# Optimization experiments

Measured on AMD Instinct MI355X. Metric: run time of the kernel, lower is better.

## Reference

```python
import jax, jax.numpy as jnp
import numpy as np

B, N, D_MODEL, H = 2, 2048, 1024, 16
HD = D_MODEL // H  # head_dim = 64

def setup_inputs() -> dict:
    key = jax.random.key(0)
    ks = jax.random.split(key, 5)
    x = jax.random.normal(ks[0], (B, N, D_MODEL), dtype=jnp.float32)
    scale = 0.02
    # Linear weights stored as [in, out] (torch does x @ W.T with W [out,in]; equivalent math)
    Wq = jax.random.normal(ks[1], (D_MODEL, D_MODEL), dtype=jnp.float32) * scale
    Wk = jax.random.normal(ks[2], (D_MODEL, D_MODEL), dtype=jnp.float32) * scale
    Wv = jax.random.normal(ks[3], (D_MODEL, D_MODEL), dtype=jnp.float32) * scale
    Wo = jax.random.normal(ks[4], (D_MODEL, D_MODEL), dtype=jnp.float32) * scale
    return {"x": x, "Wq": Wq, "Wk": Wk, "Wv": Wv, "Wo": Wo}

def reference(x, Wq, Wk, Wv, Wo):
    b, n, _ = x.shape
    # QKV projections (no bias; qkv_bias=False)
    q = (x @ Wq).reshape(b, n, H, HD)
    k = (x @ Wk).reshape(b, n, H, HD)
    v = (x @ Wv).reshape(b, n, H, HD)
    # scores [b, h, q, k]
    scores = jnp.einsum('bqhd,bkhd->bhqk', q, k) / jnp.sqrt(jnp.float32(HD))
    causal = jnp.triu(jnp.ones((n, n), dtype=bool), k=1)  # True above diagonal -> masked
    scores = jnp.where(causal, -jnp.inf, scores)
    attn = jax.nn.softmax(scores, axis=-1)  # dropout p=0.0 -> identity
    ctx = jnp.einsum('bhqk,bkhd->bqhd', attn, v).reshape(b, n, D_MODEL)
    return ctx @ Wo
```

## Files before the change

kernel.cpp:

```cpp
#include <hip/hip_runtime.h>
#include <math.h>

#define D_MODEL 1024
#define NHEAD 16
#define HD 64
#define SEQ 2048
#define BATCH 2
#define MTOT (BATCH * SEQ)

typedef __attribute__((ext_vector_type(8))) short bf16x8;
typedef __attribute__((ext_vector_type(4))) float f32x4;

__device__ __forceinline__ unsigned short f2bf(float f) {
    unsigned int u = __float_as_uint(f);
    u += 0x7FFF + ((u >> 16) & 1);
    return (unsigned short)(u >> 16);
}

__device__ __forceinline__ unsigned int pk2bf(float a, float b) {
    unsigned int r;
    asm("v_cvt_pk_bf16_f32 %0, %1, %2" : "=v"(r) : "v"(a), "v"(b));
    return r;
}

__device__ __forceinline__ void async16(unsigned short* lds, const unsigned short* g) {
    __builtin_amdgcn_global_load_lds(
        (const __attribute__((address_space(1))) unsigned int*)g,
        (__attribute__((address_space(3))) unsigned int*)lds, 16, 0, 0);
}

__device__ __forceinline__ void BAR() {
    asm volatile("" ::: "memory");
    __builtin_amdgcn_s_barrier();
    asm volatile("" ::: "memory");
}

__global__ __launch_bounds__(256) void prep(const float* __restrict__ x,
                                            unsigned short* __restrict__ xb,
                                            const float* __restrict__ W0,
                                            const float* __restrict__ W1,
                                            const float* __restrict__ W2,
                                            const float* __restrict__ W3,
                                            unsigned short* __restrict__ Wt) {
    const int bid = blockIdx.x;
    const int tid = threadIdx.x;
    if (bid < 4096) {
        const int i = (bid * 256 + tid) * 4;
        float4 v = *(const float4*)(x + i);
        uint2 pk;
        pk.x = pk2bf(v.x, v.y);
        pk.y = pk2bf(v.z, v.w);
        *(uint2*)(xb + i) = pk;
    } else {
        __shared__ float T[32][33];
        const int t = bid - 4096;
        const int z = t >> 10, rem = t & 1023;
        const int n0 = (rem & 31) * 32, k0 = (rem >> 5) * 32;
        const float* W = (z == 0) ? W0 : (z == 1) ? W1 : (z == 2) ? W2 : W3;
        unsigned short* out = Wt + (size_t)z * D_MODEL * D_MODEL;
        const int tx = tid & 31, ty = tid >> 5;
#pragma unroll
        for (int i = 0; i < 4; ++i)
            T[ty + 8 * i][tx] = W[(size_t)(k0 + ty + 8 * i) * D_MODEL + n0 + tx];
        __syncthreads();
#pragma unroll
        for (int i = 0; i < 4; ++i)
            out[(size_t)(n0 + ty + 8 * i) * D_MODEL + k0 + tx] = f2bf(T[tx][ty + 8 * i]);
    }
}

__global__ __launch_bounds__(512, 2) void qkv_mfma(const unsigned short* __restrict__ A,
                                                   const unsigned short* __restrict__ Wt,
                                                   unsigned short* __restrict__ q,
                                                   unsigned short* __restrict__ k,
                                                   unsigned short* __restrict__ vt) {
    __shared__ unsigned short SM[65536];
    const int tid = threadIdx.x;
    const int wave = tid >> 6, lane = tid & 63;
    const int quad = lane >> 4, l16 = lane & 15;
    const int wm = wave >> 2, wn = wave & 3;

    const int bid = blockIdx.x;
    const int swz = (bid & 7) * 24 + (bid >> 3);
    const int by = swz / 12, bx = swz % 12;
    const int m0 = by * 256;
    const int z = bx >> 2, c0 = (bx & 3) * 256;
    const unsigned short* Bz = Wt + (size_t)z * D_MODEL * D_MODEL;

    const unsigned short* aptr[2];
    const unsigned short* bptr[2];
    int ldsoff[2];
#pragma unroll
    for (int j = 0; j < 2; ++j) {
        const int s = j * 512 + tid;
        const int r = s >> 2;
        const int cg = (s & 3) ^ ((r + (r >> 2)) & 3);
        aptr[j] = A + (size_t)(m0 + r) * D_MODEL + cg * 8;
        bptr[j] = Bz + (size_t)(c0 + r) * D_MODEL + cg * 8;
        ldsoff[j] = (j * 512 + wave * 64) * 8;
    }

    const int key = (l16 + (l16 >> 2)) & 3;
    const int chunk = quad ^ key;
    int aoff[8], boff[4];
#pragma unroll
    for (int mt = 0; mt < 8; ++mt)
        aoff[mt] = ((wm * 128 + mt * 16 + l16) * 4 + chunk) * 8;
#pragma unroll
    for (int nt = 0; nt < 4; ++nt)
        boff[nt] = 16384 + ((wn * 64 + nt * 16 + l16) * 4 + chunk) * 8;

    f32x4 acc[8][4];
#pragma unroll
    for (int mt = 0; mt < 8; ++mt)
#pragma unroll
        for (int nt = 0; nt < 4; ++nt)
            acc[mt][nt] = (f32x4){0.f, 0.f, 0.f, 0.f};

    auto stage = [&](int d, int op, int ks, int T) {
        const int base = d * 32768 + op * 16384 + ks * 8192;
#pragma unroll
        for (int j = 0; j < 2; ++j)
            async16(SM + base + ldsoff[j],
                    (op ? bptr[j] : aptr[j]) + T * 64 + ks * 32);
    };
    auto dsA = [&](bf16x8* af, int mh, int d, int ks) {
        const int base = d * 32768 + ks * 8192;
#pragma unroll
        for (int i = 0; i < 4; ++i)
            af[i] = *(const bf16x8*)&SM[base + aoff[mh * 4 + i]];
    };
    auto dsB = [&](bf16x8* bf, int d, int ks) {
        const int base = d * 32768 + ks * 8192;
#pragma unroll
        for (int i = 0; i < 4; ++i)
            bf[i] = *(const bf16x8*)&SM[base + boff[i]];
    };
    auto mfma16 = [&](bf16x8* af, bf16x8* bf, int mh) {
        __builtin_amdgcn_s_setprio(1);
#pragma unroll
        for (int i = 0; i < 4; ++i)
#pragma unroll
            for (int nt = 0; nt < 4; ++nt)
                acc[mh * 4 + i][nt] = __builtin_amdgcn_mfma_f32_16x16x32_bf16(
                    af[i], bf[nt], acc[mh * 4 + i][nt], 0, 0, 0);
        __builtin_amdgcn_s_setprio(0);
    };

    stage(0, 0, 0, 0);
    stage(0, 1, 0, 0);
    stage(0, 0, 1, 0);
    stage(0, 1, 1, 0);
    asm volatile("s_waitcnt vmcnt(4)" ::: "memory");
    BAR();

    const int NT = D_MODEL / 64;
    for (int T = 0; T < NT; ++T) {
        const int d = T & 1, dn = d ^ 1;
        const bool nx = (T + 1 < NT);
        bf16x8 af[4], bf[4];
        if (nx) stage(dn, 0, 0, T + 1);
        dsA(af, 0, d, 0);
        dsB(bf, d, 0);
        mfma16(af, bf, 0);
        BAR();
        if (nx) stage(dn, 1, 0, T + 1);
        dsA(af, 1, d, 0);
        mfma16(af, bf, 1);
        if (nx) asm volatile("s_waitcnt vmcnt(4)" ::: "memory");
        else    asm volatile("s_waitcnt vmcnt(0)" ::: "memory");
        BAR();
        if (nx) stage(dn, 0, 1, T + 1);
        dsA(af, 0, d, 1);
        dsB(bf, d, 1);
        mfma16(af, bf, 0);
        BAR();
        if (nx) stage(dn, 1, 1, T + 1);
        dsA(af, 1, d, 1);
        mfma16(af, bf, 1);
        if (nx) asm volatile("s_waitcnt vmcnt(4)" ::: "memory");
        else    asm volatile("s_waitcnt vmcnt(0)" ::: "memory");
        BAR();
    }

    __syncthreads();
    const int bb = m0 >> 11, tok0 = m0 & (SEQ - 1), h0 = c0 >> 6;
    if (z < 2) {
        const float qsc = (z == 0) ? 0.18033688011112042f : 1.0f;
        unsigned short* dst = (z == 0) ? q : k;
#pragma unroll
        for (int pass = 0; pass < 2; ++pass) {
            if (pass) __syncthreads();
            if (wm == pass) {
#pragma unroll
                for (int mt = 0; mt < 8; ++mt)
#pragma unroll
                    for (int nt = 0; nt < 4; ++nt)
#pragma unroll
                        for (int reg = 0; reg < 4; ++reg) {
                            const int rr = mt * 16 + quad * 4 + reg;
                            const int cc = wn * 64 + nt * 16 + l16;
                            SM[rr * 264 + cc] = f2bf(acc[mt][nt][reg] * qsc);
                        }
            }
            __syncthreads();
#pragma unroll
            for (int it = 0; it < 8; ++it) {
                const int g = it * 512 + tid;
                const int r = g >> 5, gg = g & 31;
                uint4 val = *(const uint4*)&SM[r * 264 + gg * 8];
                *(uint4*)(dst + (((size_t)bb * NHEAD + h0 + (gg >> 3)) * SEQ +
                                 tok0 + pass * 128 + r) * HD + (gg & 7) * 8) = val;
            }
        }
    } else {
#pragma unroll
        for (int pass = 0; pass < 2; ++pass) {
            if (pass) __syncthreads();
            if (wm == pass) {
#pragma unroll
                for (int mt = 0; mt < 8; ++mt)
#pragma unroll
                    for (int nt = 0; nt < 4; ++nt) {
                        const int dd = wn * 64 + nt * 16 + l16;
                        const int m = mt * 16 + quad * 4;
                        uint2 w;
                        w.x = pk2bf(acc[mt][nt][0], acc[mt][nt][1]);
                        w.y = pk2bf(acc[mt][nt][2], acc[mt][nt][3]);
                        *(uint2*)&SM[dd * 136 + m] = w;
                    }
            }
            __syncthreads();
#pragma unroll
            for (int it = 0; it < 8; ++it) {
                const int g = it * 512 + tid;
                const int dd = g >> 4, tg = (g & 15) * 8;
                uint4 val = *(const uint4*)&SM[dd * 136 + tg];
                *(uint4*)(vt + (((size_t)bb * NHEAD + h0 + (dd >> 6)) * HD + (dd & 63)) * SEQ +
                          tok0 + pass * 128 + tg) = val;
            }
        }
    }
}

__global__ __launch_bounds__(256) void gemm_out(const unsigned short* __restrict__ A,
                                                const unsigned short* __restrict__ Bw,
                                                float* __restrict__ outf) {
    __shared__ unsigned short SM[16384];
    const int tid = threadIdx.x;
    const int m0 = blockIdx.y * 128, n0 = blockIdx.x * 128;
    const int wave = tid >> 6, lane = tid & 63;
    const int quad = lane >> 4, l16 = lane & 15;
    const int wm = wave & 1, wn = wave >> 1;

    f32x4 acc[4][4];
#pragma unroll
    for (int mt = 0; mt < 4; ++mt)
#pragma unroll
        for (int nt = 0; nt < 4; ++nt)
            acc[mt][nt] = (f32x4){0.f, 0.f, 0.f, 0.f};

    for (int k0 = 0; k0 < D_MODEL; k0 += 64) {
        __syncthreads();
#pragma unroll
        for (int i = 0; i < 4; ++i) {
            const int c = i * 256 + tid;
            const int r = c >> 3, cc = (c & 7) * 8;
            const int cbase = i * 256 + wave * 64;
            async16(SM + cbase * 8, A + (size_t)(m0 + r) * D_MODEL + k0 + cc);
            async16(SM + 8192 + cbase * 8, Bw + (size_t)(n0 + r) * D_MODEL + k0 + cc);
        }
        __syncthreads();
#pragma unroll
        for (int ks = 0; ks < 2; ++ks) {
            bf16x8 af[4], bfr[4];
#pragma unroll
            for (int mt = 0; mt < 4; ++mt)
                af[mt] = *(const bf16x8*)&SM[(wm * 64 + mt * 16 + l16) * 64 + ks * 32 + quad * 8];
#pragma unroll
            for (int nt = 0; nt < 4; ++nt)
                bfr[nt] = *(const bf16x8*)&SM[8192 + (wn * 64 + nt * 16 + l16) * 64 + ks * 32 + quad * 8];
#pragma unroll
            for (int mt = 0; mt < 4; ++mt)
#pragma unroll
                for (int nt = 0; nt < 4; ++nt)
                    acc[mt][nt] = __builtin_amdgcn_mfma_f32_16x16x32_bf16(
                        af[mt], bfr[nt], acc[mt][nt], 0, 0, 0);
        }
    }

#pragma unroll
    for (int mt = 0; mt < 4; ++mt)
#pragma unroll
        for (int nt = 0; nt < 4; ++nt)
#pragma unroll
            for (int reg = 0; reg < 4; ++reg) {
                const int m = m0 + wm * 64 + mt * 16 + quad * 4 + reg;
                const int n = n0 + wn * 64 + nt * 16 + l16;
                outf[(size_t)m * D_MODEL + n] = acc[mt][nt][reg];
            }
}

__global__ __launch_bounds__(256, 2) void attn_mfma(const unsigned short* __restrict__ Q,
                                                    const unsigned short* __restrict__ K,
                                                    const unsigned short* __restrict__ VT,
                                                    unsigned short* __restrict__ ctx) {
    __shared__ float CMB[8832];
    const int tid = threadIdx.x;
    const int wave = tid >> 6, lane = tid & 63;
    const int quad = lane >> 4, l16 = lane & 15;
    const int h = blockIdx.x, b = blockIdx.z;
    const int y = blockIdx.y;
    const unsigned short* Qp = Q + ((size_t)b * NHEAD + h) * SEQ * HD;
    const unsigned short* Kp = K + ((size_t)b * NHEAD + h) * SEQ * HD;
    const unsigned short* Vp = VT + ((size_t)b * NHEAD + h) * HD * SEQ;
    unsigned short* Pw = (unsigned short*)CMB + wave * 4096;
    const int sw8 = l16 & 7;

#pragma unroll 1
    for (int half = 0; half < 2; ++half) {
        const int p = half ? y : (31 - y);
        const int row0 = p * 64;
        if (half) __syncthreads();

        bf16x8 bQ[4][2];
#pragma unroll
        for (int f = 0; f < 4; ++f)
#pragma unroll
            for (int ks = 0; ks < 2; ++ks)
                bQ[f][ks] = *(const bf16x8*)(Qp +
                    (size_t)(row0 + f * 16 + l16) * HD + ks * 32 + quad * 8);

        f32x4 o[4][4];
        float ps[4] = {0.f, 0.f, 0.f, 0.f};
#pragma unroll
        for (int nt = 0; nt < 4; ++nt)
#pragma unroll
            for (int f = 0; f < 4; ++f)
                o[nt][f] = (f32x4){0.f, 0.f, 0.f, 0.f};

        for (int kt = wave; kt <= p; kt += 4) {
            bf16x8 aK[4][2];
#pragma unroll
            for (int mt = 0; mt < 4; ++mt)
#pragma unroll
                for (int ks = 0; ks < 2; ++ks)
                    aK[mt][ks] = *(const bf16x8*)(Kp +
                        (size_t)(kt * 64 + mt * 16 + l16) * HD + ks * 32 + quad * 8);

            f32x4 sT[4][4];
            __builtin_amdgcn_s_setprio(1);
#pragma unroll
            for (int mt = 0; mt < 4; ++mt)
#pragma unroll
                for (int f = 0; f < 4; ++f) {
                    sT[mt][f] = __builtin_amdgcn_mfma_f32_16x16x32_bf16(
                        aK[mt][0], bQ[f][0], (f32x4){0.f, 0.f, 0.f, 0.f}, 0, 0, 0);
                    sT[mt][f] = __builtin_amdgcn_mfma_f32_16x16x32_bf16(
                        aK[mt][1], bQ[f][1], sT[mt][f], 0, 0, 0);
                }
            __builtin_amdgcn_s_setprio(0);

            bf16x8 aV[4][2];
#pragma unroll
            for (int nt = 0; nt < 4; ++nt)
#pragma unroll
                for (int ks = 0; ks < 2; ++ks)
                    aV[nt][ks] = *(const bf16x8*)(Vp +
                        (size_t)(nt * 16 + l16) * SEQ + kt * 64 + ks * 32 + quad * 8);

            const bool diag = (kt == p);
#pragma unroll
            for (int mt = 0; mt < 4; ++mt)
#pragma unroll
                for (int f = 0; f < 4; ++f) {
                    float pv[4];
#pragma unroll
                    for (int reg = 0; reg < 4; ++reg)
                        pv[reg] = __builtin_amdgcn_exp2f(sT[mt][f][reg]);
                    if (diag) {
                        const int kb = kt * 64 + mt * 16 + quad * 4;
                        const int qg = row0 + f * 16 + l16;
#pragma unroll
                        for (int reg = 0; reg < 4; ++reg)
                            pv[reg] = (kb + reg > qg) ? 0.f : pv[reg];
                    }
                    ps[f] += (pv[0] + pv[1]) + (pv[2] + pv[3]);
                    uint2 w;
                    w.x = pk2bf(pv[0], pv[1]);
                    w.y = pk2bf(pv[2], pv[3]);
                    const int gph = ((mt * 2 + (quad >> 1)) ^ sw8);
                    *(uint2*)&Pw[(f * 16 + l16) * 64 + gph * 8 + (quad & 1) * 4] = w;
                }

            bf16x8 bP[4][2];
#pragma unroll
            for (int f = 0; f < 4; ++f)
#pragma unroll
                for (int ks = 0; ks < 2; ++ks)
                    bP[f][ks] = *(const bf16x8*)&Pw[(f * 16 + l16) * 64 +
                                                    ((ks * 4 + quad) ^ sw8) * 8];

            __builtin_amdgcn_s_setprio(1);
#pragma unroll
            for (int nt = 0; nt < 4; ++nt)
#pragma unroll
                for (int f = 0; f < 4; ++f) {
                    o[nt][f] = __builtin_amdgcn_mfma_f32_16x16x32_bf16(
                        aV[nt][0], bP[f][0], o[nt][f], 0, 0, 0);
                    o[nt][f] = __builtin_amdgcn_mfma_f32_16x16x32_bf16(
                        aV[nt][1], bP[f][1], o[nt][f], 0, 0, 0);
                }
            __builtin_amdgcn_s_setprio(0);
        }

#pragma unroll
        for (int f = 0; f < 4; ++f) {
            ps[f] += __shfl_xor(ps[f], 16);
            ps[f] += __shfl_xor(ps[f], 32);
        }

        __syncthreads();
        if (wave >= 2) {
            float* Rg = CMB + (wave - 2) * 4352;
#pragma unroll
            for (int nt = 0; nt < 4; ++nt)
#pragma unroll
                for (int f = 0; f < 4; ++f)
                    *(f32x4*)&Rg[(f * 16 + l16) * 68 + nt * 16 + quad * 4] = o[nt][f];
            if (quad == 0)
#pragma unroll
                for (int f = 0; f < 4; ++f)
                    CMB[8704 + (wave - 2) * 64 + f * 16 + l16] = ps[f];
        }
        __syncthreads();
        if (wave < 2) {
            float* Rg = CMB + wave * 4352;
#pragma unroll
            for (int nt = 0; nt < 4; ++nt)
#pragma unroll
                for (int f = 0; f < 4; ++f)
                    o[nt][f] += *(const f32x4*)&Rg[(f * 16 + l16) * 68 + nt * 16 + quad * 4];
#pragma unroll
            for (int f = 0; f < 4; ++f)
                ps[f] += CMB[8704 + wave * 64 + f * 16 + l16];
        }
        __syncthreads();
        if (wave == 1) {
#pragma unroll
            for (int nt = 0; nt < 4; ++nt)
#pragma unroll
                for (int f = 0; f < 4; ++f)
                    *(f32x4*)&CMB[(f * 16 + l16) * 68 + nt * 16 + quad * 4] = o[nt][f];
            if (quad == 0)
#pragma unroll
                for (int f = 0; f < 4; ++f)
                    CMB[8704 + f * 16 + l16] = ps[f];
        }
        __syncthreads();
        if (wave == 0) {
#pragma unroll
            for (int nt = 0; nt < 4; ++nt)
#pragma unroll
                for (int f = 0; f < 4; ++f)
                    o[nt][f] += *(const f32x4*)&CMB[(f * 16 + l16) * 68 + nt * 16 + quad * 4];
            float inv[4];
#pragma unroll
            for (int f = 0; f < 4; ++f)
                inv[f] = 1.f / (ps[f] + CMB[8704 + f * 16 + l16]);
#pragma unroll
            for (int nt = 0; nt < 4; ++nt)
#pragma unroll
                for (int f = 0; f < 4; ++f) {
                    const int tok = row0 + f * 16 + l16;
                    const int col = h * HD + nt * 16 + quad * 4;
                    uint2 w;
                    w.x = pk2bf(o[nt][f][0] * inv[f], o[nt][f][1] * inv[f]);
                    w.y = pk2bf(o[nt][f][2] * inv[f], o[nt][f][3] * inv[f]);
                    *(uint2*)(ctx + ((size_t)b * SEQ + tok) * D_MODEL + col) = w;
                }
        }
    }
}

extern "C" void kernel_launch(void* const* d_in, const int* in_sizes, int n_in,
                              void* d_out, int out_size, void* d_ws, size_t ws_size,
                              hipStream_t stream) {
    const float* x  = (const float*)d_in[0];
    const float* Wq = (const float*)d_in[1];
    const float* Wk = (const float*)d_in[2];
    const float* Wv = (const float*)d_in[3];
    const float* Wo = (const float*)d_in[4];
    float* out = (float*)d_out;

    unsigned short* ws = (unsigned short*)d_ws;
    const size_t T = (size_t)MTOT * D_MODEL;
    unsigned short* xb  = ws;
    unsigned short* Wt  = ws + T;
    unsigned short* q   = ws + 2 * T;
    unsigned short* k   = ws + 3 * T;
    unsigned short* vt  = ws + 4 * T;
    unsigned short* ctx = ws + 5 * T;

    prep<<<dim3(8192), dim3(256), 0, stream>>>(x, xb, Wq, Wk, Wv, Wo, Wt);

    qkv_mfma<<<dim3(192), dim3(512), 0, stream>>>(xb, Wt, q, k, vt);

    attn_mfma<<<dim3(NHEAD, 16, BATCH), dim3(256), 0, stream>>>(q, k, vt, ctx);

    gemm_out<<<dim3(8, 32), dim3(256), 0, stream>>>(ctx, Wt + 3 * (size_t)D_MODEL * D_MODEL, out);
}
```

Measured before the change: 182.4 us.

## Retile QKV GEMM to 256x192 tiles so grid fills all CUs

The fused QKV projection now uses 256x192 output tiles spanning the concatenated 3072-wide Q/K/V weight, launching 256 blocks instead of 192 so the 256 CUs on the device are all occupied. B-tile staging, LDS layout, wait counts and the epilogue are reworked for 48-column wave slices, and the epilogue handles tiles that straddle Q/K/V boundaries by processing three 64-column head groups. In exchange, each block does less MFMA work per A-tile load, which lowers arithmetic intensity, and the epilogue adds extra barriers.

Result: no change. 180.0 us (-1.3%).

```diff
diff --git a/kernel.cpp b/kernel.cpp
--- a/kernel.cpp
+++ b/kernel.cpp
@@ -74,170 +74,184 @@
                                                    unsigned short* __restrict__ q,
                                                    unsigned short* __restrict__ k,
                                                    unsigned short* __restrict__ vt) {
-    __shared__ unsigned short SM[65536];
+    __shared__ unsigned short SM[57344];
     const int tid = threadIdx.x;
     const int wave = tid >> 6, lane = tid & 63;
     const int quad = lane >> 4, l16 = lane & 15;
     const int wm = wave >> 2, wn = wave & 3;
 
     const int bid = blockIdx.x;
-    const int swz = (bid & 7) * 24 + (bid >> 3);
-    const int by = swz / 12, bx = swz % 12;
+    const int swz = (bid & 7) * 32 + (bid >> 3);
+    const int by = swz >> 4, bx = swz & 15;
     const int m0 = by * 256;
-    const int z = bx >> 2, c0 = (bx & 3) * 256;
-    const unsigned short* Bz = Wt + (size_t)z * D_MODEL * D_MODEL;
+    const int c0 = bx * 192;
+    const unsigned short* Bz = Wt;
 
     const unsigned short* aptr[2];
     const unsigned short* bptr[2];
-    int ldsoff[2];
 #pragma unroll
     for (int j = 0; j < 2; ++j) {
         const int s = j * 512 + tid;
         const int r = s >> 2;
         const int cg = (s & 3) ^ ((r + (r >> 2)) & 3);
         aptr[j] = A + (size_t)(m0 + r) * D_MODEL + cg * 8;
-        bptr[j] = Bz + (size_t)(c0 + r) * D_MODEL + cg * 8;
-        ldsoff[j] = (j * 512 + wave * 64) * 8;
+        const int rb = (r < 192) ? r : 191;
+        bptr[j] = Bz + (size_t)(c0 + rb) * D_MODEL + cg * 8;
     }
+    const int ldsA0 = (wave * 64) * 8, ldsA1 = (512 + wave * 64) * 8;
+    const int ldsB0 = (wave * 64) * 8, ldsB1 = (512 + wave * 64) * 8;
 
     const int key = (l16 + (l16 >> 2)) & 3;
     const int chunk = quad ^ key;
-    int aoff[8], boff[4];
+    int aoff[8], boff[3];
 #pragma unroll
     for (int mt = 0; mt < 8; ++mt)
         aoff[mt] = ((wm * 128 + mt * 16 + l16) * 4 + chunk) * 8;
 #pragma unroll
-    for (int nt = 0; nt < 4; ++nt)
-        boff[nt] = 16384 + ((wn * 64 + nt * 16 + l16) * 4 + chunk) * 8;
-
-    f32x4 acc[8][4];
+    for (int nt = 0; nt < 3; ++nt)
+        boff[nt] = ((wn * 48 + nt * 16 + l16) * 4 + chunk) * 8;
+
+    f32x4 acc[8][3];
 #pragma unroll
     for (int mt = 0; mt < 8; ++mt)
 #pragma unroll
-        for (int nt = 0; nt < 4; ++nt)
+        for (int nt = 0; nt < 3; ++nt)
             acc[mt][nt] = (f32x4){0.f, 0.f, 0.f, 0.f};
 
-    auto stage = [&](int d, int op, int ks, int T) {
-        const int base = d * 32768 + op * 16384 + ks * 8192;
-#pragma unroll
-        for (int j = 0; j < 2; ++j)
-            async16(SM + base + ldsoff[j],
-                    (op ? bptr[j] : aptr[j]) + T * 64 + ks * 32);
+    auto stageA = [&](int d, int ks, int T) {
+        const int base = d * 28672 + ks * 8192;
+        async16(SM + base + ldsA0, aptr[0] + T * 64 + ks * 32);
+        async16(SM + base + ldsA1, aptr[1] + T * 64 + ks * 32);
+    };
+    auto stageB = [&](int d, int ks, int T) {
+        const int base = d * 28672 + 16384 + ks * 6144;
+        async16(SM + base + ldsB0, bptr[0] + T * 64 + ks * 32);
+        if (wave < 4)
+            async16(SM + base + ldsB1, bptr[1] + T * 64 + ks * 32);
     };
     auto dsA = [&](bf16x8* af, int mh, int d, int ks) {
-        const int base = d * 32768 + ks * 8192;
+        const int base = d * 28672 + ks * 8192;
 #pragma unroll
         for (int i = 0; i < 4; ++i)
             af[i] = *(const bf16x8*)&SM[base + aoff[mh * 4 + i]];
     };
     auto dsB = [&](bf16x8* bf, int d, int ks) {
-        const int base = d * 32768 + ks * 8192;
-#pragma unroll
-        for (int i = 0; i < 4; ++i)
+        const int base = d * 28672 + 16384 + ks * 6144;
+#pragma unroll
+        for (int i = 0; i < 3; ++i)
             bf[i] = *(const bf16x8*)&SM[base + boff[i]];
     };
-    auto mfma16 = [&](bf16x8* af, bf16x8* bf, int mh) {
+    auto mfma12 = [&](bf16x8* af, bf16x8* bf, int mh) {
         __builtin_amdgcn_s_setprio(1);
 #pragma unroll
         for (int i = 0; i < 4; ++i)
 #pragma unroll
-            for (int nt = 0; nt < 4; ++nt)
+            for (int nt = 0; nt < 3; ++nt)
                 acc[mh * 4 + i][nt] = __builtin_amdgcn_mfma_f32_16x16x32_bf16(
                     af[i], bf[nt], acc[mh * 4 + i][nt], 0, 0, 0);
         __builtin_amdgcn_s_setprio(0);
     };
-
-    stage(0, 0, 0, 0);
-    stage(0, 1, 0, 0);
-    stage(0, 0, 1, 0);
-    stage(0, 1, 1, 0);
-    asm volatile("s_waitcnt vmcnt(4)" ::: "memory");
+    auto waitc = [&](bool nx) {
+        if (nx) {
+            if (wave < 4) asm volatile("s_waitcnt vmcnt(4)" ::: "memory");
+            else          asm volatile("s_waitcnt vmcnt(3)" ::: "memory");
+        } else {
+            asm volatile("s_waitcnt vmcnt(0)" ::: "memory");
+        }
+    };
+
+    stageA(0, 0, 0);
+    stageB(0, 0, 0);
+    stageA(0, 1, 0);
+    stageB(0, 1, 0);
+    waitc(true);
     BAR();
 
     const int NT = D_MODEL / 64;
     for (int T = 0; T < NT; ++T) {
         const int d = T & 1, dn = d ^ 1;
         const bool nx = (T + 1 < NT);
-        bf16x8 af[4], bf[4];
-        if (nx) stage(dn, 0, 0, T + 1);
+        bf16x8 af[4], bf[3];
+        if (nx) stageA(dn, 0, T + 1);
         dsA(af, 0, d, 0);
         dsB(bf, d, 0);
-        mfma16(af, bf, 0);
+        mfma12(af, bf, 0);
         BAR();
-        if (nx) stage(dn, 1, 0, T + 1);
+        if (nx) stageB(dn, 0, T + 1);
         dsA(af, 1, d, 0);
-        mfma16(af, bf, 1);
-        if (nx) asm volatile("s_waitcnt vmcnt(4)" ::: "memory");
-        else    asm volatile("s_waitcnt vmcnt(0)" ::: "memory");
+        mfma12(af, bf, 1);
+        waitc(nx);
         BAR();
-        if (nx) stage(dn, 0, 1, T + 1);
+        if (nx) stageA(dn, 1, T + 1);
         dsA(af, 0, d, 1);
         dsB(bf, d, 1);
-        mfma16(af, bf, 0);
+        mfma12(af, bf, 0);
         BAR();
-        if (nx) stage(dn, 1, 1, T + 1);
+        if (nx) stageB(dn, 1, T + 1);
         dsA(af, 1, d, 1);
-        mfma16(af, bf, 1);
-        if (nx) asm volatile("s_waitcnt vmcnt(4)" ::: "memory");
-        else    asm volatile("s_waitcnt vmcnt(0)" ::: "memory");
+        mfma12(af, bf, 1);
+        waitc(nx);
         BAR();
     }
 
     __syncthreads();
-    const int bb = m0 >> 11, tok0 = m0 & (SEQ - 1), h0 = c0 >> 6;
-    if (z < 2) {
-        const float qsc = (z == 0) ? 0.18033688011112042f : 1.0f;
-        unsigned short* dst = (z == 0) ? q : k;
-#pragma unroll
-        for (int pass = 0; pass < 2; ++pass) {
-            if (pass) __syncthreads();
-            if (wm == pass) {
-#pragma unroll
-                for (int mt = 0; mt < 8; ++mt)
-#pragma unroll
-                    for (int nt = 0; nt < 4; ++nt)
+    const int bb = m0 >> 11, tok0 = m0 & (SEQ - 1);
+#pragma unroll 1
+    for (int G = 0; G < 3; ++G) {
+        if (G) __syncthreads();
+        const int gcol = c0 + G * 64;
+        const int zg = gcol >> 10;
+        const int hg = (gcol >> 6) & 15;
+        if (zg < 2) {
+            const float sc = (zg == 0) ? 0.18033688011112042f : 1.0f;
+            unsigned short* dst = (zg == 0) ? q : k;
+#pragma unroll
+            for (int nt = 0; nt < 3; ++nt) {
+                const int colb = wn * 48 + nt * 16;
+                if ((colb >> 6) == G) {
+                    const int cl = colb - G * 64 + l16;
+#pragma unroll
+                    for (int mt = 0; mt < 8; ++mt)
 #pragma unroll
                         for (int reg = 0; reg < 4; ++reg) {
-                            const int rr = mt * 16 + quad * 4 + reg;
-                            const int cc = wn * 64 + nt * 16 + l16;
-                            SM[rr * 264 + cc] = f2bf(acc[mt][nt][reg] * qsc);
+                            const int rr = wm * 128 + mt * 16 + quad * 4 + reg;
+                            SM[rr * 64 + cl] = f2bf(acc[mt][nt][reg] * sc);
                         }
+                }
             }
             __syncthreads();
 #pragma unroll
-            for (int it = 0; it < 8; ++it) {
+            for (int it = 0; it < 4; ++it) {
                 const int g = it * 512 + tid;
-                const int r = g >> 5, gg = g & 31;
-                uint4 val = *(const uint4*)&SM[r * 264 + gg * 8];
-                *(uint4*)(dst + (((size_t)bb * NHEAD + h0 + (gg >> 3)) * SEQ +
-                                 tok0 + pass * 128 + r) * HD + (gg & 7) * 8) = val;
+                const int r = g >> 3, c8 = g & 7;
+                uint4 val = *(const uint4*)&SM[r * 64 + c8 * 8];
+                *(uint4*)(dst + (((size_t)bb * NHEAD + hg) * SEQ + tok0 + r) * HD +
+                          c8 * 8) = val;
             }
-        }
-    } else {
-#pragma unroll
-        for (int pass = 0; pass < 2; ++pass) {
-            if (pass) __syncthreads();
-            if (wm == pass) {
-#pragma unroll
-                for (int mt = 0; mt < 8; ++mt)
-#pragma unroll
-                    for (int nt = 0; nt < 4; ++nt) {
-                        const int dd = wn * 64 + nt * 16 + l16;
-                        const int m = mt * 16 + quad * 4;
+        } else {
+#pragma unroll
+            for (int nt = 0; nt < 3; ++nt) {
+                const int colb = wn * 48 + nt * 16;
+                if ((colb >> 6) == G) {
+                    const int dl = colb - G * 64 + l16;
+#pragma unroll
+                    for (int mt = 0; mt < 8; ++mt) {
+                        const int m = wm * 128 + mt * 16 + quad * 4;
                         uint2 w;
                         w.x = pk2bf(acc[mt][nt][0], acc[mt][nt][1]);
                         w.y = pk2bf(acc[mt][nt][2], acc[mt][nt][3]);
-                        *(uint2*)&SM[dd * 136 + m] = w;
+                        *(uint2*)&SM[dl * 264 + m] = w;
                     }
+                }
             }
             __syncthreads();
 #pragma unroll
-            for (int it = 0; it < 8; ++it) {
+            for (int it = 0; it < 4; ++it) {
                 const int g = it * 512 + tid;
-                const int dd = g >> 4, tg = (g & 15) * 8;
-                uint4 val = *(const uint4*)&SM[dd * 136 + tg];
-                *(uint4*)(vt + (((size_t)bb * NHEAD + h0 + (dd >> 6)) * HD + (dd & 63)) * SEQ +
-                          tok0 + pass * 128 + tg) = val;
+                const int dd = g >> 5, t8 = (g & 31) * 8;
+                uint4 val = *(const uint4*)&SM[dd * 264 + t8];
+                *(uint4*)(vt + (((size_t)bb * NHEAD + hg) * HD + dd) * SEQ + tok0 +
+                          t8) = val;
             }
         }
     }
@@ -504,7 +518,7 @@
 
     prep<<<dim3(8192), dim3(256), 0, stream>>>(x, xb, Wq, Wk, Wv, Wo, Wt);
 
-    qkv_mfma<<<dim3(192), dim3(512), 0, stream>>>(xb, Wt, q, k, vt);
+    qkv_mfma<<<dim3(256), dim3(512), 0, stream>>>(xb, Wt, q, k, vt);
 
     attn_mfma<<<dim3(NHEAD, 16, BATCH), dim3(256), 0, stream>>>(q, k, vt, ctx);
 
```
